# Optimization experiments

Hardware: AMD Instinct MI355X
Metric: run time of the kernel (lower is better)

The kernel has to match this reference:

```python
import jax, jax.numpy as jnp
import numpy as np

OFFS = [[0, -1], [-1, 0], [-1, -1], [0, -2], [-2, 0], [-2, -2], [0, -3], [-3, 0], [-3, -3]]
SIGMA = 1.2  # module's self.sigma; overseg_factor == 1.0 so the aff scaling is a no-op


def _gauss_kernel(sigma, truncate=4.0):
    # matches scipy/skimage gaussian: radius = int(truncate*sigma + 0.5)
    r = int(truncate * sigma + 0.5)
    t = np.arange(-r, r + 1)
    k = np.exp(-0.5 * (t / sigma) ** 2)
    return jnp.asarray(k / k.sum(), jnp.float32), r


def _blur_axis(x, k, r, axis):
    # x: [C,H,W]; skimage default mode='nearest' -> edge padding
    pad = [(0, 0)] * x.ndim
    pad[axis] = (r, r)
    xp = jnp.pad(x, pad, mode='edge')
    n = x.shape[axis]
    out = k[0] * jax.lax.slice_in_dim(xp, 0, n, axis=axis)
    for i in range(1, 2 * r + 1):
        out = out + k[i] * jax.lax.slice_in_dim(xp, i, i + n, axis=axis)
    return out


def gaussian_blur(x, sigma):
    k, r = _gauss_kernel(sigma)
    return _blur_axis(_blur_axis(x, k, r, 1), k, r, 2)


def naive_affinities(raw, offs):
    # per-offset intensity-difference affinity, normalized by its max
    affs = []
    for off in offs:
        rolled = jnp.roll(raw, (-off[0], -off[1]), axis=(-2, -1))
        d = jnp.sqrt(((raw - rolled) ** 2).sum(0))  # norm over channel dim
        affs.append(d / d.max())
    return jnp.stack(affs)  # [9,H,W]


def setup_inputs() -> dict:
    key = jax.random.key(0)
    k1, k2, k3, k4 = jax.random.split(key, 4)
    B, E, H, W = 4, 32, 512, 512
    return {
        'embeds': jax.random.normal(k1, (B, E, H, W), jnp.float32),
        'tf_embeds': jax.random.normal(k2, (B, E, H, W), jnp.float32),
        'raw': jax.random.uniform(k3, (1, 1, H, W), jnp.float32),
        'mask': jax.random.uniform(k4, (1, 9, H, W), jnp.float32),
    }


def reference(embeds, tf_embeds, raw, mask):
    r = raw[0]      # [C,H,W]
    m = mask[0]     # [9,H,W]
    affs = naive_affinities(gaussian_blur(r, SIGMA), OFFS)
    # sep_chnl scaling with overseg_factor=1.0 is identity; clamp as in torch
    affs = jnp.clip(affs, 0.0, 1.0)
    loss = jnp.zeros((), embeds.dtype)
    for i, off in enumerate(OFFS):
        rolled = jnp.roll(tf_embeds, (-off[0], -off[1]), axis=(-2, -1))
        dist = (1.0 - (embeds * rolled).sum(1)) * m[i][None]  # [B,H,W]
        a = affs[i] - affs[i].min()
        a = a / a.max()
        loss = loss + (dist * (0.5 - a)[None]).mean()
    return loss
```

## Files before the change

kernel.cpp:

```cpp
#include <hip/hip_runtime.h>
#include <math.h>

#define Hh 512
#define Ww 512
#define Bb 4
#define Ee 32
#define PLANE (Hh*Ww)
#define NOFF 9

#define WS_BLUR   0
#define WS_TMP    262144
#define WS_KW     524288
#define WS_MIN    524304
#define WS_MAX    524320
#define WS_ACC    524336

__global__ void k_init(float* ws){
    int t = threadIdx.x;
    unsigned int* mn = (unsigned int*)(ws + WS_MIN);
    unsigned int* mx = (unsigned int*)(ws + WS_MAX);
    if (t < 16){ mn[t] = 0x7F800000u; mx[t] = 0u; }
    if (t == 0){
        *(double*)(ws + WS_ACC) = 0.0;
        double k[11], s = 0.0;
        for (int i = 0; i < 11; i++){
            double x = (double)(i - 5) / 1.2;
            k[i] = exp(-0.5 * x * x);
            s += k[i];
        }
        for (int i = 0; i < 11; i++) ws[WS_KW + i] = (float)(k[i] / s);
    }
}

__global__ void k_blur_h(const float* __restrict__ raw, float* __restrict__ ws){
    int idx = blockIdx.x * 256 + threadIdx.x;
    int h = idx >> 9, w = idx & 511;
    float acc = 0.f;
    #pragma unroll
    for (int i = 0; i < 11; i++){
        int hh = h + i - 5;
        hh = hh < 0 ? 0 : (hh > Hh-1 ? Hh-1 : hh);
        acc += ws[WS_KW + i] * raw[hh * Ww + w];
    }
    ws[WS_TMP + idx] = acc;
}

__global__ void k_blur_w(float* __restrict__ ws){
    int idx = blockIdx.x * 256 + threadIdx.x;
    int h = idx >> 9, w = idx & 511;
    float acc = 0.f;
    #pragma unroll
    for (int i = 0; i < 11; i++){
        int wwi = w + i - 5;
        wwi = wwi < 0 ? 0 : (wwi > Ww-1 ? Ww-1 : wwi);
        acc += ws[WS_KW + i] * ws[WS_TMP + h * Ww + wwi];
    }
    ws[WS_BLUR + idx] = acc;
}

__device__ __constant__ int d_OH[NOFF] = {0,-1,-1,0,-2,-2,0,-3,-3};
__device__ __constant__ int d_OW[NOFF] = {-1,0,-1,-2,0,-2,-3,0,-3};

__global__ void k_minmax(float* __restrict__ ws){
    int idx = blockIdx.x * 512 + threadIdx.x;
    int h = idx >> 9, w = idx & 511;
    float bc = ws[WS_BLUR + idx];
    int lane = threadIdx.x & 63, wv = threadIdx.x >> 6;
    __shared__ float smn[8 * NOFF], smx[8 * NOFF];
    #pragma unroll
    for (int i = 0; i < NOFF; i++){
        int hn = (h + d_OH[i]) & (Hh-1);
        int wn = (w + d_OW[i]) & (Ww-1);
        float d = fabsf(bc - ws[WS_BLUR + hn * Ww + wn]);
        float mnv = d, mxv = d;
        for (int s = 32; s; s >>= 1){
            mnv = fminf(mnv, __shfl_xor(mnv, s));
            mxv = fmaxf(mxv, __shfl_xor(mxv, s));
        }
        if (lane == 0){ smn[wv * NOFF + i] = mnv; smx[wv * NOFF + i] = mxv; }
    }
    __syncthreads();
    if (threadIdx.x < NOFF){
        float mnv = smn[threadIdx.x], mxv = smx[threadIdx.x];
        for (int v = 1; v < 8; v++){
            mnv = fminf(mnv, smn[v * NOFF + threadIdx.x]);
            mxv = fmaxf(mxv, smx[v * NOFF + threadIdx.x]);
        }
        atomicMin((unsigned int*)(ws + WS_MIN) + threadIdx.x, __float_as_uint(mnv));
        atomicMax((unsigned int*)(ws + WS_MAX) + threadIdx.x, __float_as_uint(mxv));
    }
}

__launch_bounds__(512)
__global__ void k_main(const float* __restrict__ E, const float* __restrict__ T,
                       const float* __restrict__ mask, float* __restrict__ ws){
    int g = blockIdx.x * 512 + threadIdx.x;
    int b  = g >> 16;
    int hr = (g >> 7) & 511;
    int wq = g & 127;
    int c0 = wq << 2;
    int cl = (c0 - 4) & 511;
    int rr0 = hr, rr1 = (hr-1)&511, rr2 = (hr-2)&511, rr3 = (hr-3)&511;
    int pix = hr * Ww + c0;

    int ro[4] = { rr0*Ww + c0, rr1*Ww + c0, rr2*Ww + c0, rr3*Ww + c0 };
    int lo[4] = { rr0*Ww + cl, rr1*Ww + cl, rr2*Ww + cl, rr3*Ww + cl };

    const float* bl = ws + WS_BLUR;
    float tb[4][8];
    #pragma unroll
    for (int r = 0; r < 4; r++){
        float4 l4 = *(const float4*)(bl + lo[r]);
        float4 o4 = *(const float4*)(bl + ro[r]);
        tb[r][0]=l4.x; tb[r][1]=l4.y; tb[r][2]=l4.z; tb[r][3]=l4.w;
        tb[r][4]=o4.x; tb[r][5]=o4.y; tb[r][6]=o4.z; tb[r][7]=o4.w;
    }
    const unsigned int* mnb = (const unsigned int*)(ws + WS_MIN);
    const unsigned int* mxb = (const unsigned int*)(ws + WS_MAX);
    float mn[NOFF], inv[NOFF];
    #pragma unroll
    for (int i = 0; i < NOFF; i++){
        mn[i]  = __uint_as_float(mnb[i]);
        inv[i] = 1.f / (__uint_as_float(mxb[i]) - mn[i]);
    }
    float mk[NOFF][4];
    #pragma unroll
    for (int i = 0; i < NOFF; i++){
        float4 m4 = *(const float4*)(mask + i * PLANE + pix);
        mk[i][0]=m4.x; mk[i][1]=m4.y; mk[i][2]=m4.z; mk[i][3]=m4.w;
    }
    float c[4][NOFF], csum[4];
    #pragma unroll
    for (int j = 0; j < 4; j++){
        float bc = tb[0][4+j];
        float d[NOFF];
        d[0] = fabsf(bc - tb[0][3+j]);
        d[1] = fabsf(bc - tb[1][4+j]);
        d[2] = fabsf(bc - tb[1][3+j]);
        d[3] = fabsf(bc - tb[0][2+j]);
        d[4] = fabsf(bc - tb[2][4+j]);
        d[5] = fabsf(bc - tb[2][2+j]);
        d[6] = fabsf(bc - tb[0][1+j]);
        d[7] = fabsf(bc - tb[3][4+j]);
        d[8] = fabsf(bc - tb[3][1+j]);
        csum[j] = 0.f;
        #pragma unroll
        for (int i = 0; i < NOFF; i++){
            float a = (d[i] - mn[i]) * inv[i];
            c[j][i] = mk[i][j] * (0.5f - a);
            csum[j] += c[j][i];
        }
    }

    const float* Eb = E + (size_t)b * Ee * PLANE + pix;
    const float* Tb = T + (size_t)b * Ee * PLANE;
    float acc[4] = {0.f, 0.f, 0.f, 0.f};
    for (int e = 0; e < Ee; e++){
        const float* Tp = Tb + (size_t)e * PLANE;
        float4 ev4 = *(const float4*)(Eb + (size_t)e * PLANE);
        float ev[4] = {ev4.x, ev4.y, ev4.z, ev4.w};
        float t[4][8];
        #pragma unroll
        for (int r = 0; r < 4; r++){
            float4 l4 = *(const float4*)(Tp + lo[r]);
            float4 o4 = *(const float4*)(Tp + ro[r]);
            t[r][0]=l4.x; t[r][1]=l4.y; t[r][2]=l4.z; t[r][3]=l4.w;
            t[r][4]=o4.x; t[r][5]=o4.y; t[r][6]=o4.z; t[r][7]=o4.w;
        }
        #pragma unroll
        for (int j = 0; j < 4; j++){
            float s =        c[j][0] * t[0][3+j];
            s = fmaf(c[j][1], t[1][4+j], s);
            s = fmaf(c[j][2], t[1][3+j], s);
            s = fmaf(c[j][3], t[0][2+j], s);
            s = fmaf(c[j][4], t[2][4+j], s);
            s = fmaf(c[j][5], t[2][2+j], s);
            s = fmaf(c[j][6], t[0][1+j], s);
            s = fmaf(c[j][7], t[3][4+j], s);
            s = fmaf(c[j][8], t[3][1+j], s);
            acc[j] = fmaf(ev[j], s, acc[j]);
        }
    }

    float part = (csum[0]-acc[0]) + (csum[1]-acc[1]) + (csum[2]-acc[2]) + (csum[3]-acc[3]);

    for (int s = 32; s; s >>= 1) part += __shfl_xor(part, s);
    __shared__ float sp[8];
    int lane = threadIdx.x & 63, wv = threadIdx.x >> 6;
    if (lane == 0) sp[wv] = part;
    __syncthreads();
    if (threadIdx.x == 0){
        float bs = 0.f;
        for (int v = 0; v < 8; v++) bs += sp[v];
        atomicAdd((double*)(ws + WS_ACC), (double)bs);
    }
}

__global__ void k_final(const float* __restrict__ ws, float* __restrict__ out){
    out[0] = (float)(*(const double*)(ws + WS_ACC) / (double)((size_t)Bb * PLANE));
}

extern "C" void kernel_launch(void* const* d_in, const int* in_sizes, int n_in,
                              void* d_out, int out_size, void* d_ws, size_t ws_size,
                              hipStream_t stream) {
    const float* embeds = (const float*)d_in[0];
    const float* tf     = (const float*)d_in[1];
    const float* raw    = (const float*)d_in[2];
    const float* mask   = (const float*)d_in[3];
    float* ws  = (float*)d_ws;
    float* out = (float*)d_out;

    k_init  <<<1, 64, 0, stream>>>(ws);
    k_blur_h<<<PLANE/256, 256, 0, stream>>>(raw, ws);
    k_blur_w<<<PLANE/256, 256, 0, stream>>>(ws);
    k_minmax<<<PLANE/512, 512, 0, stream>>>(ws);
    k_main  <<<PLANE*Bb/4/512, 512, 0, stream>>>(embeds, tf, mask, ws);
    k_final <<<1, 1, 0, stream>>>(ws, out);
}
```

Measured before the change: 92.01 us.

## Fuse blur passes and init into one tiled kernel, fold final into main

Replaces the init kernel and the two separable blur kernels with one shared-memory tiled blur kernel that computes the Gaussian weights itself and also initializes the min/max/accumulator buffers. Removes the final kernel by having the last k_main block, detected with a completion counter, write the output. k_main moves to 256-thread blocks with launch bounds set for occupancy, and the mask values are read inside the coefficient loop instead of being preloaded. The goal is fewer kernel launches and fewer intermediate global round-trips, in exchange for a completion atomic and scalar mask loads.

After: 128.7 us. 1.4x slower.

```diff
diff --git a/kernel.cpp b/kernel.cpp
--- a/kernel.cpp
+++ b/kernel.cpp
@@ -9,57 +9,67 @@
 #define NOFF 9
 
 #define WS_BLUR   0
-#define WS_TMP    262144
-#define WS_KW     524288
 #define WS_MIN    524304
 #define WS_MAX    524320
 #define WS_ACC    524336
-
-__global__ void k_init(float* ws){
-    int t = threadIdx.x;
-    unsigned int* mn = (unsigned int*)(ws + WS_MIN);
-    unsigned int* mx = (unsigned int*)(ws + WS_MAX);
-    if (t < 16){ mn[t] = 0x7F800000u; mx[t] = 0u; }
-    if (t == 0){
-        *(double*)(ws + WS_ACC) = 0.0;
-        double k[11], s = 0.0;
-        for (int i = 0; i < 11; i++){
-            double x = (double)(i - 5) / 1.2;
-            k[i] = exp(-0.5 * x * x);
-            s += k[i];
-        }
-        for (int i = 0; i < 11; i++) ws[WS_KW + i] = (float)(k[i] / s);
-    }
-}
-
-__global__ void k_blur_h(const float* __restrict__ raw, float* __restrict__ ws){
-    int idx = blockIdx.x * 256 + threadIdx.x;
-    int h = idx >> 9, w = idx & 511;
-    float acc = 0.f;
-    #pragma unroll
-    for (int i = 0; i < 11; i++){
-        int hh = h + i - 5;
-        hh = hh < 0 ? 0 : (hh > Hh-1 ? Hh-1 : hh);
-        acc += ws[WS_KW + i] * raw[hh * Ww + w];
-    }
-    ws[WS_TMP + idx] = acc;
-}
-
-__global__ void k_blur_w(float* __restrict__ ws){
-    int idx = blockIdx.x * 256 + threadIdx.x;
-    int h = idx >> 9, w = idx & 511;
-    float acc = 0.f;
-    #pragma unroll
-    for (int i = 0; i < 11; i++){
-        int wwi = w + i - 5;
-        wwi = wwi < 0 ? 0 : (wwi > Ww-1 ? Ww-1 : wwi);
-        acc += ws[WS_KW + i] * ws[WS_TMP + h * Ww + wwi];
-    }
-    ws[WS_BLUR + idx] = acc;
-}
+#define WS_CNT    524338
 
 __device__ __constant__ int d_OH[NOFF] = {0,-1,-1,0,-2,-2,0,-3,-3};
 __device__ __constant__ int d_OW[NOFF] = {-1,0,-1,-2,0,-2,-3,0,-3};
+
+#define TS 32
+#define HALO 5
+__global__ __launch_bounds__(256) void k_blur(const float* __restrict__ raw,
+                                              float* __restrict__ ws){
+    __shared__ float sraw[TS+2*HALO][TS+2*HALO+1];
+    __shared__ float shb [TS][TS+2*HALO+1];
+    int tx = blockIdx.x & 15, ty = blockIdx.x >> 4;
+    int r0 = ty*TS - HALO, c0 = tx*TS - HALO;
+
+    double kd[11], s = 0.0;
+    #pragma unroll
+    for (int i = 0; i < 11; i++){
+        double x = (double)(i - 5) / 1.2;
+        kd[i] = exp(-0.5 * x * x);
+        s += kd[i];
+    }
+    float w[11];
+    #pragma unroll
+    for (int i = 0; i < 11; i++) w[i] = (float)(kd[i] / s);
+
+    for (int t = threadIdx.x; t < 42*42; t += 256){
+        int rr = t / 42, cc = t - rr*42;
+        int gr = min(max(r0+rr, 0), Hh-1);
+        int gc = min(max(c0+cc, 0), Ww-1);
+        sraw[rr][cc] = raw[gr*Ww + gc];
+    }
+    __syncthreads();
+    for (int t = threadIdx.x; t < TS*42; t += 256){
+        int rr = t / 42, cc = t - rr*42;
+        float a = 0.f;
+        #pragma unroll
+        for (int i = 0; i < 11; i++) a += w[i] * sraw[rr+i][cc];
+        shb[rr][cc] = a;
+    }
+    __syncthreads();
+    for (int t = threadIdx.x; t < TS*TS; t += 256){
+        int rr = t >> 5, cc = t & 31;
+        float a = 0.f;
+        #pragma unroll
+        for (int i = 0; i < 11; i++) a += w[i] * shb[rr][cc+i];
+        ws[WS_BLUR + (ty*TS+rr)*Ww + (tx*TS+cc)] = a;
+    }
+    if (blockIdx.x == 0){
+        if (threadIdx.x < 16){
+            ((unsigned int*)(ws + WS_MIN))[threadIdx.x] = 0x7F800000u;
+            ((unsigned int*)(ws + WS_MAX))[threadIdx.x] = 0u;
+        }
+        if (threadIdx.x == 0){
+            *(double*)(ws + WS_ACC) = 0.0;
+            *(unsigned int*)(ws + WS_CNT) = 0u;
+        }
+    }
+}
 
 __global__ void k_minmax(float* __restrict__ ws){
     int idx = blockIdx.x * 512 + threadIdx.x;
@@ -91,20 +101,21 @@
     }
 }
 
-__launch_bounds__(512)
-__global__ void k_main(const float* __restrict__ E, const float* __restrict__ T,
-                       const float* __restrict__ mask, float* __restrict__ ws){
-    int g = blockIdx.x * 512 + threadIdx.x;
+__global__ __launch_bounds__(256, 4)
+void k_main(const float* __restrict__ E, const float* __restrict__ T,
+            const float* __restrict__ mask, float* __restrict__ ws,
+            float* __restrict__ out){
+    int g = blockIdx.x * 256 + threadIdx.x;
     int b  = g >> 16;
     int hr = (g >> 7) & 511;
     int wq = g & 127;
     int c0 = wq << 2;
     int cl = (c0 - 4) & 511;
-    int rr0 = hr, rr1 = (hr-1)&511, rr2 = (hr-2)&511, rr3 = (hr-3)&511;
+    int rr1 = (hr-1)&511, rr2 = (hr-2)&511, rr3 = (hr-3)&511;
     int pix = hr * Ww + c0;
 
-    int ro[4] = { rr0*Ww + c0, rr1*Ww + c0, rr2*Ww + c0, rr3*Ww + c0 };
-    int lo[4] = { rr0*Ww + cl, rr1*Ww + cl, rr2*Ww + cl, rr3*Ww + cl };
+    int ro[4] = { pix,           rr1*Ww + c0, rr2*Ww + c0, rr3*Ww + c0 };
+    int lo[4] = { hr*Ww + cl,    rr1*Ww + cl, rr2*Ww + cl, rr3*Ww + cl };
 
     const float* bl = ws + WS_BLUR;
     float tb[4][8];
@@ -123,13 +134,8 @@
         mn[i]  = __uint_as_float(mnb[i]);
         inv[i] = 1.f / (__uint_as_float(mxb[i]) - mn[i]);
     }
-    float mk[NOFF][4];
-    #pragma unroll
-    for (int i = 0; i < NOFF; i++){
-        float4 m4 = *(const float4*)(mask + i * PLANE + pix);
-        mk[i][0]=m4.x; mk[i][1]=m4.y; mk[i][2]=m4.z; mk[i][3]=m4.w;
-    }
-    float c[4][NOFF], csum[4];
+    float c[4][NOFF];
+    float acc[4];
     #pragma unroll
     for (int j = 0; j < 4; j++){
         float bc = tb[0][4+j];
@@ -143,18 +149,20 @@
         d[6] = fabsf(bc - tb[0][1+j]);
         d[7] = fabsf(bc - tb[3][4+j]);
         d[8] = fabsf(bc - tb[3][1+j]);
-        csum[j] = 0.f;
+        acc[j] = 0.f;
+        float4 dummy;
         #pragma unroll
         for (int i = 0; i < NOFF; i++){
             float a = (d[i] - mn[i]) * inv[i];
-            c[j][i] = mk[i][j] * (0.5f - a);
-            csum[j] += c[j][i];
-        }
+            float mv = ((const float*)(mask + i * PLANE + pix))[j];
+            c[j][i] = mv * (0.5f - a);
+            acc[j] += c[j][i];
+        }
+        (void)dummy;
     }
 
     const float* Eb = E + (size_t)b * Ee * PLANE + pix;
     const float* Tb = T + (size_t)b * Ee * PLANE;
-    float acc[4] = {0.f, 0.f, 0.f, 0.f};
     for (int e = 0; e < Ee; e++){
         const float* Tp = Tb + (size_t)e * PLANE;
         float4 ev4 = *(const float4*)(Eb + (size_t)e * PLANE);
@@ -178,26 +186,28 @@
             s = fmaf(c[j][6], t[0][1+j], s);
             s = fmaf(c[j][7], t[3][4+j], s);
             s = fmaf(c[j][8], t[3][1+j], s);
-            acc[j] = fmaf(ev[j], s, acc[j]);
-        }
-    }
-
-    float part = (csum[0]-acc[0]) + (csum[1]-acc[1]) + (csum[2]-acc[2]) + (csum[3]-acc[3]);
+            acc[j] = fmaf(-ev[j], s, acc[j]);
+        }
+    }
+
+    float part = acc[0] + acc[1] + acc[2] + acc[3];
 
     for (int s = 32; s; s >>= 1) part += __shfl_xor(part, s);
-    __shared__ float sp[8];
+    __shared__ float sp[4];
     int lane = threadIdx.x & 63, wv = threadIdx.x >> 6;
     if (lane == 0) sp[wv] = part;
     __syncthreads();
     if (threadIdx.x == 0){
-        float bs = 0.f;
-        for (int v = 0; v < 8; v++) bs += sp[v];
-        atomicAdd((double*)(ws + WS_ACC), (double)bs);
-    }
-}
-
-__global__ void k_final(const float* __restrict__ ws, float* __restrict__ out){
-    out[0] = (float)(*(const double*)(ws + WS_ACC) / (double)((size_t)Bb * PLANE));
+        float bs = sp[0] + sp[1] + sp[2] + sp[3];
+        double* accp = (double*)(ws + WS_ACC);
+        atomicAdd(accp, (double)bs);
+        __threadfence();
+        unsigned int done = atomicAdd((unsigned int*)(ws + WS_CNT), 1u);
+        if (done == gridDim.x - 1){
+            double v = atomicAdd(accp, 0.0);
+            out[0] = (float)(v / (double)((size_t)Bb * PLANE));
+        }
+    }
 }
 
 extern "C" void kernel_launch(void* const* d_in, const int* in_sizes, int n_in,
@@ -210,10 +220,7 @@
     float* ws  = (float*)d_ws;
     float* out = (float*)d_out;
 
-    k_init  <<<1, 64, 0, stream>>>(ws);
-    k_blur_h<<<PLANE/256, 256, 0, stream>>>(raw, ws);
-    k_blur_w<<<PLANE/256, 256, 0, stream>>>(ws);
+    k_blur  <<<256, 256, 0, stream>>>(raw, ws);
     k_minmax<<<PLANE/512, 512, 0, stream>>>(ws);
-    k_main  <<<PLANE*Bb/4/512, 512, 0, stream>>>(embeds, tf, mask, ws);
-    k_final <<<1, 1, 0, stream>>>(ws, out);
-}
+    k_main  <<<PLANE*Bb/4/256, 256, 0, stream>>>(embeds, tf, mask, ws, out);
+}
```
